# Optimization experiments

Hardware: AMD Instinct MI355X
Metric: run time of the kernel (lower is better)

Reference implementation:

```python
import jax, jax.numpy as jnp
import numpy as np
from jax import lax

E = 20          # num experts / classes
BN_EPS = 1e-5


def _conv(x, w, b=None):
    # NCHW conv, stride 1, 'same' padding (kernel 3x3 or 1x1)
    y = lax.conv_general_dilated(x, w, (1, 1), 'SAME',
                                 dimension_numbers=('NCHW', 'OIHW', 'NCHW'))
    return y if b is None else y + b[None, :, None, None]


def _lrelu(x):
    return jnp.where(x >= 0, x, 0.2 * x)


def _bn(x, g, b, m, v):
    # inference-mode batchnorm
    scale = g * lax.rsqrt(v + BN_EPS)
    return x * scale[None, :, None, None] + (b - m * scale)[None, :, None, None]


def setup_inputs() -> dict:
    key = jax.random.key(0)
    ks = iter(jax.random.split(key, 40))
    def w(shape):
        return jax.random.normal(next(ks), shape, jnp.float32) * 0.05
    d = {}
    d['x'] = jax.random.normal(next(ks), (2, 3, 192, 192), jnp.float32)
    d['noise'] = jax.random.normal(next(ks), (2, 128, 192, 192), jnp.float32)
    # classification head
    d['cls_w1'] = w((64, 3, 3, 3));    d['cls_b1'] = jnp.zeros((64,), jnp.float32)
    d['cls_w2'] = w((128, 64, 3, 3));  d['cls_b2'] = jnp.zeros((128,), jnp.float32)
    d['cls_w3'] = w((256, 128, 3, 3)); d['cls_b3'] = jnp.zeros((256,), jnp.float32)
    d['cls_w4'] = w((512, 256, 1, 1)); d['cls_b4'] = jnp.zeros((512,), jnp.float32)
    d['cls_w5'] = w((E, 512, 1, 1));   d['cls_b5'] = jnp.zeros((E,), jnp.float32)
    for c, i in ((128, 1), (256, 2), (512, 3)):
        d[f'bn{i}_g'] = jnp.ones((c,), jnp.float32)
        d[f'bn{i}_b'] = jnp.zeros((c,), jnp.float32)
        d[f'bn{i}_m'] = jnp.zeros((c,), jnp.float32)
        d[f'bn{i}_v'] = jnp.ones((c,), jnp.float32)
    # 20 expert encoders (stacked on leading axis)
    d['enc_w1'] = w((E, 32, 3, 3, 3));    d['enc_b1'] = jnp.zeros((E, 32), jnp.float32)
    d['enc_w2'] = w((E, 64, 32, 3, 3));   d['enc_b2'] = jnp.zeros((E, 64), jnp.float32)
    d['enc_w3'] = w((E, 128, 64, 3, 3));  d['enc_b3'] = jnp.zeros((E, 128), jnp.float32)
    d['enc_w4'] = w((E, 128, 128, 3, 3)); d['enc_b4'] = jnp.zeros((E, 128), jnp.float32)
    # decoder (legacy=False: first two 1x1 convs have no bias)
    d['dec_w1'] = w((64, 128, 1, 1))
    d['dec_w2'] = w((32, 64, 1, 1))
    d['dec_w3'] = w((3, 32, 1, 1)); d['dec_b3'] = jnp.zeros((3,), jnp.float32)
    return d


def reference(x, noise,
              cls_w1, cls_b1, cls_w2, cls_b2, cls_w3, cls_b3,
              cls_w4, cls_b4, cls_w5, cls_b5,
              bn1_g, bn1_b, bn1_m, bn1_v,
              bn2_g, bn2_b, bn2_m, bn2_v,
              bn3_g, bn3_b, bn3_m, bn3_v,
              enc_w1, enc_b1, enc_w2, enc_b2, enc_w3, enc_b3, enc_w4, enc_b4,
              dec_w1, dec_w2, dec_w3, dec_b3):
    B, _, H, W = x.shape
    C = enc_w4.shape[1]  # 128
    # --- classification / routing ---
    h = _lrelu(_conv(x, cls_w1, cls_b1))
    h = _lrelu(_bn(_conv(h, cls_w2, cls_b2), bn1_g, bn1_b, bn1_m, bn1_v))
    h = _lrelu(_bn(_conv(h, cls_w3, cls_b3), bn2_g, bn2_b, bn2_m, bn2_v))
    h = _lrelu(_bn(_conv(h, cls_w4, cls_b4), bn3_g, bn3_b, bn3_m, bn3_v))
    classes = jax.nn.softmax(_conv(h, cls_w5, cls_b5), axis=1)  # [B,E,H,W]
    idx = jnp.argmax(classes, axis=1)  # [B,H,W] top-1 expert per pixel

    # --- run all 20 dense encoders (faithful to original torch.where masking) ---
    def enc(w1, b1, w2, b2, w3, b3, w4, b4):
        e = _lrelu(_conv(x, w1, b1))
        e = _lrelu(_conv(e, w2, b2))
        e = _lrelu(_conv(e, w3, b3))
        return _conv(e, w4, b4)
    embs = jax.vmap(enc)(enc_w1, enc_b1, enc_w2, enc_b2,
                         enc_w3, enc_b3, enc_w4, enc_b4)  # [E,B,128,H,W]
    embs = jnp.moveaxis(embs, 0, 1)  # [B,E,128,H,W]
    sel_idx = jnp.broadcast_to(idx[:, None, None, :, :], (B, 1, C, H, W))
    emb = jnp.take_along_axis(embs, sel_idx, axis=1)[:, 0]  # [B,128,H,W]

    # --- decode with additive noise ---
    d = _conv(emb + noise, dec_w1)
    d = _conv(d, dec_w2)
    out = _conv(d, dec_w3, dec_b3)  # [B,3,H,W]

    # --- load balancing loss ---
    one_hot = jax.nn.one_hot(idx, E, dtype=jnp.float32)          # [B,H,W,E]
    density = one_hot.reshape(B, -1, E).mean(axis=1)             # [B,E]
    density_proxy = classes.reshape(B, E, -1).mean(axis=-1)      # [B,E]
    lb = (density_proxy * density).mean() * float(E * E)
    return out, lb * 0.1
```

## Files before the change

### kernel.cpp

```cpp
#include <hip/hip_runtime.h>
#include <hip/hip_bf16.h>

typedef __hip_bfloat16 bf16;
typedef unsigned short u16;
typedef short s16x8 __attribute__((ext_vector_type(8)));
typedef float f32x4 __attribute__((ext_vector_type(4)));
#define MFMA16(a, b, c) __builtin_amdgcn_mfma_f32_16x16x32_bf16(a, b, c, 0, 0, 0)

#define HW_   36864
#define WP_   194
#define HWP_  37636
#define W_    192
#define SP_   9216

__device__ __forceinline__ float ldin(const void* p, size_t i, int f32) {
    return f32 ? ((const float*)p)[i] : __bfloat162float(((const bf16*)p)[i]);
}
__device__ __forceinline__ int probe_f32(const void* pr) {
    return ((const unsigned*)pr)[0] == 0x3F800000u;
}
__device__ __forceinline__ u16 f2bf(float f) {
    bf16 h = __float2bfloat16(f);
    return *reinterpret_cast<u16*>(&h);
}

__global__ __launch_bounds__(256) void pad_x_k(const void* __restrict__ x,
                                               float* __restrict__ xpad,
                                               const void* __restrict__ pr) {
    const int f32 = probe_f32(pr);
    int i = blockIdx.x * 256 + threadIdx.x;
    if (i >= 2 * 3 * HW_) return;
    int w = i % W_;
    int h = (i / W_) % W_;
    int c = i / HW_;
    xpad[(size_t)c * HWP_ + (size_t)(h + 1) * WP_ + (w + 1)] = ldin(x, i, f32);
}

__global__ __launch_bounds__(256) void conv3x3_k(
    const float* __restrict__ in, const void* __restrict__ wgt,
    const void* __restrict__ bias, const void* __restrict__ bng,
    const void* __restrict__ bnb, const void* __restrict__ bnm,
    const void* __restrict__ bnv, float* __restrict__ out,
    int Cin, int Cout, int lrelu, const void* __restrict__ pr)
{
    extern __shared__ float wl[];
    const int f32 = probe_f32(pr);
    const int tid = threadIdx.x;
    const int co0 = blockIdx.y * 8;
    const int b   = blockIdx.z;
    const int n = Cin * 72;
    for (int i = tid; i < n; i += 256) {
        int u = i & 7, r = i >> 3;
        int ci = r / 9, tap = r - ci * 9;
        wl[i] = ldin(wgt, ((size_t)(co0 + u) * Cin + ci) * 9 + tap, f32);
    }
    __syncthreads();

    const int pixb = blockIdx.x * 1024 + tid;
    int off[4];
#pragma unroll
    for (int p = 0; p < 4; ++p) {
        int pix = pixb + p * 256;
        int h = pix / W_, w = pix - h * W_;
        off[p] = (h + 1) * WP_ + (w + 1);
    }
    float acc[32];
#pragma unroll
    for (int i = 0; i < 32; ++i) acc[i] = 0.f;

    const int doff[9] = {-(WP_+1), -WP_, -(WP_-1), -1, 0, 1, WP_-1, WP_, WP_+1};
    const float* inb = in + (size_t)b * Cin * HWP_;
    for (int ci = 0; ci < Cin; ++ci) {
        const float* ip = inb + (size_t)ci * HWP_;
        const float* wp = wl + ci * 72;
#pragma unroll
        for (int tap = 0; tap < 9; ++tap) {
            const float4 wa = *(const float4*)(wp + tap * 8);
            const float4 wb = *(const float4*)(wp + tap * 8 + 4);
            const int d = doff[tap];
            float v[4];
#pragma unroll
            for (int p = 0; p < 4; ++p) v[p] = ip[off[p] + d];
#pragma unroll
            for (int p = 0; p < 4; ++p) {
                acc[p*8+0] += v[p] * wa.x;  acc[p*8+1] += v[p] * wa.y;
                acc[p*8+2] += v[p] * wa.z;  acc[p*8+3] += v[p] * wa.w;
                acc[p*8+4] += v[p] * wb.x;  acc[p*8+5] += v[p] * wb.y;
                acc[p*8+6] += v[p] * wb.z;  acc[p*8+7] += v[p] * wb.w;
            }
        }
    }

#pragma unroll
    for (int u = 0; u < 8; ++u) {
        const int co = co0 + u;
        float s = 1.f, t = 0.f;
        if (bng) {
            float g = ldin(bng, co, f32), bb = ldin(bnb, co, f32);
            float m = ldin(bnm, co, f32), vv = ldin(bnv, co, f32);
            s = g * rsqrtf(vv + 1e-5f);
            t = bb - m * s;
        }
        const float bs = bias ? ldin(bias, co, f32) : 0.f;
        float* op = out + ((size_t)b * Cout + co) * HWP_;
#pragma unroll
        for (int p = 0; p < 4; ++p) {
            float val = (acc[p*8+u] + bs) * s + t;
            if (lrelu) val = val >= 0.f ? val : 0.2f * val;
            op[off[p]] = val;
        }
    }
}

__global__ __launch_bounds__(256) void conv1x1s_k(
    const float* __restrict__ in, const void* __restrict__ wgt,
    const void* __restrict__ bias, const void* __restrict__ bng,
    const void* __restrict__ bnb, const void* __restrict__ bnm,
    const void* __restrict__ bnv, float* __restrict__ out,
    int Cin, int pix0, const void* __restrict__ pr)
{
    extern __shared__ float wl[];
    const int f32 = probe_f32(pr);
    const int tid = threadIdx.x;
    const int co0 = blockIdx.y * 8;
    const int b   = blockIdx.z;
    const int n = Cin * 8;
    for (int i = tid; i < n; i += 256) {
        int u = i & 7, ci = i >> 3;
        wl[i] = ldin(wgt, (size_t)(co0 + u) * Cin + ci, f32);
    }
    __syncthreads();

    const int pixb = pix0 + blockIdx.x * 1024 + tid;
    int off[4], lp[4];
#pragma unroll
    for (int p = 0; p < 4; ++p) {
        int pix = pixb + p * 256;
        lp[p] = pix - pix0;
        int h = pix / W_, w = pix - h * W_;
        off[p] = (h + 1) * WP_ + (w + 1);
    }
    float acc[32];
#pragma unroll
    for (int i = 0; i < 32; ++i) acc[i] = 0.f;

    for (int ci = 0; ci < Cin; ++ci) {
        const float* ip = in + ((size_t)b * Cin + ci) * HWP_;
        const float4 wa = *(const float4*)(wl + ci * 8);
        const float4 wb = *(const float4*)(wl + ci * 8 + 4);
        float v[4];
#pragma unroll
        for (int p = 0; p < 4; ++p) v[p] = ip[off[p]];
#pragma unroll
        for (int p = 0; p < 4; ++p) {
            acc[p*8+0] += v[p] * wa.x;  acc[p*8+1] += v[p] * wa.y;
            acc[p*8+2] += v[p] * wa.z;  acc[p*8+3] += v[p] * wa.w;
            acc[p*8+4] += v[p] * wb.x;  acc[p*8+5] += v[p] * wb.y;
            acc[p*8+6] += v[p] * wb.z;  acc[p*8+7] += v[p] * wb.w;
        }
    }

#pragma unroll
    for (int u = 0; u < 8; ++u) {
        const int co = co0 + u;
        float g = ldin(bng, co, f32), bb = ldin(bnb, co, f32);
        float m = ldin(bnm, co, f32), vv = ldin(bnv, co, f32);
        float s = g * rsqrtf(vv + 1e-5f);
        float t = bb - m * s;
        const float bs = ldin(bias, co, f32);
        float* op = out + ((size_t)b * 512 + co) * SP_;
#pragma unroll
        for (int p = 0; p < 4; ++p) {
            float val = (acc[p*8+u] + bs) * s + t;
            val = val >= 0.f ? val : 0.2f * val;
            op[lp[p]] = val;
        }
    }
}

__global__ __launch_bounds__(256) void heads_k(
    const float* __restrict__ c4q, const void* __restrict__ w5,
    const void* __restrict__ b5, int* __restrict__ idx,
    float* __restrict__ proxy, float* __restrict__ cntg, int pix0,
    const void* __restrict__ pr)
{
    extern __shared__ float wl[];
    __shared__ float sums[20];
    __shared__ float cnts[20];
    const int f32 = probe_f32(pr);
    const int tid = threadIdx.x;
    const int b = blockIdx.y;
    for (int i = tid; i < 512 * 20; i += 256) {
        int e = i % 20, ci = i / 20;
        wl[ci * 20 + e] = ldin(w5, (size_t)e * 512 + ci, f32);
    }
    if (tid < 20) { sums[tid] = 0.f; cnts[tid] = 0.f; }
    __syncthreads();

    const int lpix = blockIdx.x * 256 + tid;

    float acc[20];
#pragma unroll
    for (int e = 0; e < 20; ++e) acc[e] = ldin(b5, e, f32);
    const float* ip = c4q + (size_t)b * 512 * SP_;
    for (int ci = 0; ci < 512; ++ci) {
        const float v = ip[(size_t)ci * SP_ + lpix];
        const float* wp = wl + ci * 20;
#pragma unroll
        for (int e = 0; e < 20; ++e) acc[e] += v * wp[e];
    }

    float m = acc[0]; int am = 0;
#pragma unroll
    for (int e = 1; e < 20; ++e) if (acc[e] > m) { m = acc[e]; am = e; }
    float prb[20], ssum = 0.f;
#pragma unroll
    for (int e = 0; e < 20; ++e) { prb[e] = expf(acc[e] - m); ssum += prb[e]; }
    const float inv = 1.f / ssum;
    idx[b * HW_ + pix0 + lpix] = am;

    const int lane = tid & 63;
#pragma unroll
    for (int e = 0; e < 20; ++e) {
        float p = prb[e] * inv;
        p += __shfl_down(p, 32); p += __shfl_down(p, 16); p += __shfl_down(p, 8);
        p += __shfl_down(p, 4);  p += __shfl_down(p, 2);  p += __shfl_down(p, 1);
        if (lane == 0) atomicAdd(&sums[e], p);
        unsigned long long bal = __ballot(am == e);
        if (lane == 0) atomicAdd(&cnts[e], (float)__popcll(bal));
    }
    __syncthreads();
    if (tid < 20) {
        atomicAdd(&proxy[b * 20 + tid], sums[tid]);
        atomicAdd(&cntg[b * 20 + tid], cnts[tid]);
    }
}

__global__ __launch_bounds__(256) void wtx_k(const void* __restrict__ w,
                                             u16* __restrict__ wt,
                                             int Cout, int Cin, int nTot,
                                             const void* __restrict__ pr) {
    const int f32 = probe_f32(pr);
    int i = blockIdx.x * 256 + threadIdx.x;
    if (i >= nTot) return;
    int ci = i % Cin; int r = i / Cin;
    int co = r % Cout; r /= Cout;
    int tap = r % 9; int e = r / 9;
    size_t src = ((size_t)(e * Cout + co) * Cin + ci) * 9 + tap;
    wt[i] = f2bf(ldin(w, src, f32));
}

__global__ __launch_bounds__(512) void fused_expert_k(
    const float* __restrict__ xpad, const int* __restrict__ idx,
    const void* __restrict__ ew1, const void* __restrict__ eb1,
    const u16* __restrict__ Wt2, const void* __restrict__ eb2,
    const u16* __restrict__ Wt3, const void* __restrict__ eb3,
    const u16* __restrict__ Wt4, const void* __restrict__ eb4,
    float* __restrict__ emb, const void* __restrict__ pr)
{
    __shared__ __align__(16) char smem_[137216];
    u16*   e2s = (u16*)smem_;
    u16*   e3s = (u16*)(smem_ + 54272);
    u16*   e1s = (u16*)(smem_ + 54272);
    float* xs  = (float*)smem_;
    float* wl1 = (float*)(smem_ + 6912);
    __shared__ int s_sel[256];
    __shared__ int s_wc[8];

    const int f32 = probe_f32(pr);
    const int tid  = threadIdx.x;
    const int lane = tid & 63, wv = tid >> 6;
    const int ml = lane & 15, q8 = (lane >> 4) * 8, m0 = (lane >> 4) * 4;
    const int b = blockIdx.y;
    const int eid = blockIdx.z;
    const int ty = blockIdx.x / 12, tx = blockIdx.x - ty * 12;
    const int Oh = ty * 16, Ow = tx * 16;

    {
        int sel = 0;
        if (tid < 256) {
            const int r = tid >> 4, c = tid & 15;
            sel = (idx[b * HW_ + (Oh + r) * W_ + (Ow + c)] == eid);
        }
        const unsigned long long m = __ballot(sel);
        if (lane == 0) s_wc[wv] = __popcll(m);
        __syncthreads();
        int cnt = 0;
#pragma unroll
        for (int w = 0; w < 8; ++w) cnt += s_wc[w];
        if (cnt == 0) return;
        int pre = 0;
        for (int w = 0; w < wv; ++w) pre += s_wc[w];
        if (sel)
            s_sel[pre + __popcll(m & ((1ull << lane) - 1ull))] = tid;
    }

    for (int i = tid; i < 24 * 24 * 3; i += 512) {
        int ch = i % 3, pxl = i / 3;
        int r = pxl / 24, c = pxl - r * 24;
        int ir = Oh - 4 + r, ic = Ow - 4 + c;
        float v = 0.f;
        if (ir >= -1 && ir < 193 && ic >= -1 && ic < 193)
            v = xpad[((size_t)b * 3 + ch) * HWP_ + (size_t)(ir + 1) * WP_ + (ic + 1)];
        xs[pxl * 3 + ch] = v;
    }
    for (int i = tid; i < 896; i += 512) {
        if (i < 864) {
            int co = i & 31, k = i >> 5;
            int ci = k / 9, tap = k - ci * 9;
            wl1[i] = ldin(ew1, (size_t)eid * 864 + ((size_t)co * 3 + ci) * 9 + tap, f32);
        } else {
            wl1[i] = ldin(eb1, (size_t)eid * 32 + (i - 864), f32);
        }
    }
    __syncthreads();

    if (tid < 484) {
        const int p = tid;
        const int r1 = p / 22, c1 = p - r1 * 22;
        const int ir = Oh - 3 + r1, ic = Ow - 3 + c1;
        const int inimg = (ir >= 0 && ir < 192 && ic >= 0 && ic < 192);
        float a1[32];
#pragma unroll
        for (int co = 0; co < 32; ++co) a1[co] = 0.f;
        if (inimg) {
#pragma unroll
            for (int ci = 0; ci < 3; ++ci)
#pragma unroll
                for (int tap = 0; tap < 9; ++tap) {
                    const int dy = tap / 3, dx = tap - dy * 3;
                    const float xv = xs[((r1 + dy) * 24 + (c1 + dx)) * 3 + ci];
                    const float* wp = wl1 + (ci * 9 + tap) * 32;
#pragma unroll
                    for (int co = 0; co < 32; ++co) a1[co] += xv * wp[co];
                }
        }
        u16 pk[32];
#pragma unroll
        for (int co = 0; co < 32; ++co) {
            float v = 0.f;
            if (inimg) {
                v = a1[co] + wl1[864 + co];
                v = v >= 0.f ? v : 0.2f * v;
            }
            pk[co] = f2bf(v);
        }
#pragma unroll
        for (int ch = 0; ch < 4; ++ch)
            *(uint4*)(e1s + ((size_t)ch * 488 + p) * 8) = ((const uint4*)pk)[ch];
    }
    __syncthreads();

    {
        const u16* Wt2e = Wt2 + (size_t)eid * 9 * 64 * 32;
        int pxv[4], r2v[4], c2v[4];
#pragma unroll
        for (int j = 0; j < 4; ++j) {
            int t = wv + 8 * j; if (t > 24) t = 24;
            int px = t * 16 + ml;
            pxv[j] = px; r2v[j] = px / 20; c2v[j] = px - (px / 20) * 20;
        }
        f32x4 acc2[4][4];
#pragma unroll
        for (int j = 0; j < 4; ++j)
#pragma unroll
            for (int n = 0; n < 4; ++n) acc2[j][n] = (f32x4){0.f,0.f,0.f,0.f};

#pragma unroll
        for (int tap = 0; tap < 9; ++tap) {
            const int dy = tap / 3, dx = tap - dy * 3;
            s16x8 aW[4];
#pragma unroll
            for (int n = 0; n < 4; ++n)
                aW[n] = *(const s16x8*)(Wt2e + ((size_t)tap * 64 + n * 16 + ml) * 32 + q8);
#pragma unroll
            for (int j = 0; j < 4; ++j) {
                const int lin = (r2v[j] + dy) * 22 + (c2v[j] + dx);
                const s16x8 bA = *(const s16x8*)(e1s + ((size_t)(q8 >> 3) * 488 + lin) * 8);
#pragma unroll
                for (int n = 0; n < 4; ++n) acc2[j][n] = MFMA16(aW[n], bA, acc2[j][n]);
            }
        }
        __syncthreads();
#pragma unroll
        for (int j = 0; j < 4; ++j) {
            const int px = pxv[j];
            const int r2 = r2v[j], c2 = c2v[j];
            const int ir = Oh - 2 + r2, ic = Ow - 2 + c2;
            const int inimg = (ir >= 0 && ir < 192 && ic >= 0 && ic < 192);
#pragma unroll
            for (int n = 0; n < 4; ++n) {
                u16 pk[4];
#pragma unroll
                for (int r = 0; r < 4; ++r) {
                    const int co = n * 16 + m0 + r;
                    float v = 0.f;
                    if (inimg) {
                        v = acc2[j][n][r] + ldin(eb2, (size_t)eid * 64 + co, f32);
                        v = v >= 0.f ? v : 0.2f * v;
                    }
                    pk[r] = f2bf(v);
                }
                const int chunk = (n * 16 + m0) >> 3;
                *(uint2*)(e2s + ((size_t)chunk * 424 + px) * 8 + (m0 & 4)) = *(const uint2*)pk;
            }
        }
    }
    __syncthreads();

    {
        const u16* Wt3e = Wt3 + (size_t)eid * 9 * 128 * 64;
        int pxv[3], r3v[3], c3v[3];
#pragma unroll
        for (int j = 0; j < 3; ++j) {
            int t = wv + 8 * j; if (t > 20) t = 20;
            int px = t * 16 + ml;
            pxv[j] = px; r3v[j] = px / 18; c3v[j] = px - (px / 18) * 18;
        }
#pragma unroll
        for (int np = 0; np < 2; ++np) {
            f32x4 acc3[3][4];
#pragma unroll
            for (int j = 0; j < 3; ++j)
#pragma unroll
                for (int n = 0; n < 4; ++n) acc3[j][n] = (f32x4){0.f,0.f,0.f,0.f};

#pragma unroll
            for (int tap = 0; tap < 9; ++tap) {
                const int dy = tap / 3, dx = tap - dy * 3;
#pragma unroll
                for (int cc = 0; cc < 2; ++cc) {
                    s16x8 aW[4];
#pragma unroll
                    for (int n = 0; n < 4; ++n) {
                        const int co = np * 64 + n * 16 + ml;
                        aW[n] = *(const s16x8*)(Wt3e + ((size_t)tap * 128 + co) * 64 + cc * 32 + q8);
                    }
                    const int chunk = cc * 4 + (q8 >> 3);
#pragma unroll
                    for (int j = 0; j < 3; ++j) {
                        const int lin = (r3v[j] + dy) * 20 + (c3v[j] + dx);
                        const s16x8 bA = *(const s16x8*)(e2s + ((size_t)chunk * 424 + lin) * 8);
#pragma unroll
                        for (int n = 0; n < 4; ++n) acc3[j][n] = MFMA16(aW[n], bA, acc3[j][n]);
                    }
                }
            }
#pragma unroll
            for (int j = 0; j < 3; ++j) {
                const int px = pxv[j];
                if (px >= 324) continue;
                const int r3 = r3v[j], c3 = c3v[j];
                const int ir = Oh - 1 + r3, ic = Ow - 1 + c3;
                const int inimg = (ir >= 0 && ir < 192 && ic >= 0 && ic < 192);
#pragma unroll
                for (int n = 0; n < 4; ++n) {
                    u16 pk[4];
#pragma unroll
                    for (int r = 0; r < 4; ++r) {
                        const int co = np * 64 + n * 16 + m0 + r;
                        float v = 0.f;
                        if (inimg) {
                            v = acc3[j][n][r] + ldin(eb3, (size_t)eid * 128 + co, f32);
                            v = v >= 0.f ? v : 0.2f * v;
                        }
                        pk[r] = f2bf(v);
                    }
                    const int chunk = (np * 64 + n * 16 + m0) >> 3;
                    *(uint2*)(e3s + ((size_t)chunk * 324 + px) * 8 + (m0 & 4)) = *(const uint2*)pk;
                }
            }
        }
    }
    __syncthreads();

    {
        const u16* Wt4e = Wt4 + (size_t)eid * 9 * 128 * 128;
        int cnt = 0;
#pragma unroll
        for (int w = 0; w < 8; ++w) cnt += s_wc[w];
        const int mtiles = (cnt + 15) >> 4;
        const int n0 = wv * 16;
        float bs[4];
#pragma unroll
        for (int r = 0; r < 4; ++r) bs[r] = ldin(eb4, (size_t)eid * 128 + n0 + m0 + r, f32);
        for (int mt = 0; mt < mtiles; ++mt) {
            const int li = mt * 16 + ml;
            const int lpx = (li < cnt) ? s_sel[li] : 0;
            const int rr = lpx >> 4, cc2 = lpx & 15;
            f32x4 acc = {0.f,0.f,0.f,0.f};
#pragma unroll
            for (int tap = 0; tap < 9; ++tap) {
                const int dy = tap / 3, dx = tap - dy * 3;
                const int lin = (rr + dy) * 18 + (cc2 + dx);
#pragma unroll
                for (int c0 = 0; c0 < 128; c0 += 32) {
                    const s16x8 bA = *(const s16x8*)(e3s + ((size_t)((c0 + q8) >> 3) * 324 + lin) * 8);
                    const s16x8 aW = *(const s16x8*)(Wt4e + ((size_t)tap * 128 + n0 + ml) * 128 + c0 + q8);
                    acc = MFMA16(aW, bA, acc);
                }
            }
            if (li < cnt) {
                const int g = (Oh + rr) * W_ + Ow + cc2;
#pragma unroll
                for (int r = 0; r < 4; ++r)
                    emb[((size_t)b * 128 + n0 + m0 + r) * HW_ + g] = acc[r] + bs[r];
            }
        }
    }
}

__global__ __launch_bounds__(256) void dec_fused_k(
    const float* __restrict__ emb, const void* __restrict__ noise,
    const void* __restrict__ dw1, const void* __restrict__ dw2,
    const void* __restrict__ dw3, const void* __restrict__ db3,
    void* __restrict__ outb, const void* __restrict__ pr)
{
    __shared__ float w1s[128 * 64];
    __shared__ float w2s[64 * 32];
    __shared__ float w3s[100];
    const int f32 = probe_f32(pr);
    const int tid = threadIdx.x;
    for (int i = tid; i < 128 * 64; i += 256) {
        int ci = i >> 6, co = i & 63;
        w1s[i] = ldin(dw1, (size_t)co * 128 + ci, f32);
    }
    for (int i = tid; i < 64 * 32; i += 256) {
        int ci = i >> 5, co = i & 31;
        w2s[i] = ldin(dw2, (size_t)co * 64 + ci, f32);
    }
    if (tid < 96) {
        int ci = tid / 3, k = tid - ci * 3;
        w3s[ci * 3 + k] = ldin(dw3, (size_t)k * 32 + ci, f32);
    }
    if (tid >= 96 && tid < 99) w3s[96 + tid - 96] = ldin(db3, tid - 96, f32);
    __syncthreads();

    const int b = blockIdx.y;
    const int pix = blockIdx.x * 256 + tid;

    float h1[64];
#pragma unroll
    for (int i = 0; i < 64; ++i) h1[i] = 0.f;
    for (int ci = 0; ci < 128; ++ci) {
        const size_t base = ((size_t)b * 128 + ci) * HW_ + pix;
        const float v = emb[base] + ldin(noise, base, f32);
        const float* wp = w1s + ci * 64;
#pragma unroll
        for (int c4 = 0; c4 < 16; ++c4) {
            const float4 w = *(const float4*)(wp + c4 * 4);
            h1[c4*4+0] += v * w.x; h1[c4*4+1] += v * w.y;
            h1[c4*4+2] += v * w.z; h1[c4*4+3] += v * w.w;
        }
    }
    float h2[32];
#pragma unroll
    for (int i = 0; i < 32; ++i) h2[i] = 0.f;
#pragma unroll
    for (int ci = 0; ci < 64; ++ci) {
        const float v = h1[ci];
        const float* wp = w2s + ci * 32;
#pragma unroll
        for (int c4 = 0; c4 < 8; ++c4) {
            const float4 w = *(const float4*)(wp + c4 * 4);
            h2[c4*4+0] += v * w.x; h2[c4*4+1] += v * w.y;
            h2[c4*4+2] += v * w.z; h2[c4*4+3] += v * w.w;
        }
    }
    float a0 = w3s[96], a1 = w3s[97], a2 = w3s[98];
#pragma unroll
    for (int ci = 0; ci < 32; ++ci) {
        const float v = h2[ci];
        a0 += v * w3s[ci * 3 + 0];
        a1 += v * w3s[ci * 3 + 1];
        a2 += v * w3s[ci * 3 + 2];
    }
    const size_t o0 = (size_t)(b * 3 + 0) * HW_ + pix;
    const size_t o1 = (size_t)(b * 3 + 1) * HW_ + pix;
    const size_t o2 = (size_t)(b * 3 + 2) * HW_ + pix;
    if (f32) {
        ((float*)outb)[o0] = a0; ((float*)outb)[o1] = a1; ((float*)outb)[o2] = a2;
    } else {
        ((bf16*)outb)[o0] = __float2bfloat16(a0);
        ((bf16*)outb)[o1] = __float2bfloat16(a1);
        ((bf16*)outb)[o2] = __float2bfloat16(a2);
    }
}

__global__ void lb_k(const float* __restrict__ proxy, const float* __restrict__ cnt,
                     void* __restrict__ out, const void* __restrict__ pr) {
    const int f32 = probe_f32(pr);
    const int t = threadIdx.x;
    const float inv = 1.0f / (float)HW_;
    float v = 0.f;
    if (t < 40) v = (proxy[t] * inv) * (cnt[t] * inv);
#pragma unroll
    for (int o = 32; o > 0; o >>= 1) v += __shfl_down(v, o);
    if (t == 0) {
        if (f32) ((float*)out)[221184] = v;
        else     ((bf16*)out)[221184] = __float2bfloat16(v);
    }
}

extern "C" void kernel_launch(void* const* d_in, const int* in_sizes, int n_in,
                              void* d_out, int out_size, void* d_ws, size_t ws_size,
                              hipStream_t stream) {
    (void)in_sizes; (void)n_in; (void)out_size; (void)ws_size;
    const void* x    = d_in[0];
    const void* noise= d_in[1];
    const void* cw1  = d_in[2];  const void* cb1 = d_in[3];
    const void* cw2  = d_in[4];  const void* cb2 = d_in[5];
    const void* cw3  = d_in[6];  const void* cb3 = d_in[7];
    const void* cw4  = d_in[8];  const void* cb4 = d_in[9];
    const void* cw5  = d_in[10]; const void* cb5 = d_in[11];
    const void* bn1g = d_in[12]; const void* bn1b = d_in[13];
    const void* bn1m = d_in[14]; const void* bn1v = d_in[15];
    const void* bn2g = d_in[16]; const void* bn2b = d_in[17];
    const void* bn2m = d_in[18]; const void* bn2v = d_in[19];
    const void* bn3g = d_in[20]; const void* bn3b = d_in[21];
    const void* bn3m = d_in[22]; const void* bn3v = d_in[23];
    const void* ew1  = d_in[24]; const void* eb1 = d_in[25];
    const void* ew2  = d_in[26]; const void* eb2 = d_in[27];
    const void* ew3  = d_in[28]; const void* eb3 = d_in[29];
    const void* ew4  = d_in[30]; const void* eb4 = d_in[31];
    const void* dw1  = d_in[32];
    const void* dw2  = d_in[33];
    const void* dw3  = d_in[34]; const void* db3 = d_in[35];
    const void* pr   = bn1v;

    char* ws = (char*)d_ws;
    constexpr size_t SZ_XPAD = (((size_t)2*3*HWP_*4) + 255) & ~(size_t)255;
    constexpr size_t O_BUF2  = SZ_XPAD;
    constexpr size_t SZ_BUF2 = (size_t)2*256*HWP_*4;
    constexpr size_t O_BUF1  = O_BUF2 + SZ_BUF2;
    constexpr size_t SZ_BUF1 = (size_t)2*128*HWP_*4;
    constexpr size_t O_IDX   = O_BUF1 + SZ_BUF1;
    constexpr size_t O_STAT  = O_IDX + (size_t)2*HW_*4;
    constexpr size_t WS_USED = O_STAT + 512;

    float* xpad  = (float*)(ws);
    float* buf2  = (float*)(ws + O_BUF2);
    int*   idx   = (int*)  (ws + O_IDX);
    float* proxy = (float*)(ws + O_STAT);
    float* cntg  = proxy + 40;

    float* c1  = buf2;
    float* c3  = buf2;
    float* c2  = (float*)(ws + O_BUF1);
    float* c4q = (float*)(ws + O_BUF1);
    float* emb = buf2;
    u16* Wt2 = (u16*)(ws + O_BUF1);
    u16* Wt3 = Wt2 + 368640;
    u16* Wt4 = Wt3 + 1474560;

    hipMemsetAsync(d_ws, 0, WS_USED, stream);

    dim3 blk(256);
    pad_x_k<<<dim3((2*3*HW_ + 255)/256), blk, 0, stream>>>(x, xpad, pr);

    conv3x3_k<<<dim3(36,  8, 2), blk,   3*288, stream>>>(xpad, cw1, cb1, nullptr,nullptr,nullptr,nullptr, c1,   3,  64, 1, pr);
    conv3x3_k<<<dim3(36, 16, 2), blk,  64*288, stream>>>(c1,   cw2, cb2, bn1g,bn1b,bn1m,bn1v,           c2,  64, 128, 1, pr);
    conv3x3_k<<<dim3(36, 32, 2), blk, 128*288, stream>>>(c2,   cw3, cb3, bn2g,bn2b,bn2m,bn2v,           c3, 128, 256, 1, pr);
    for (int s = 0; s < 4; ++s) {
        conv1x1s_k<<<dim3(9, 64, 2), blk, 256*32, stream>>>(c3, cw4, cb4, bn3g,bn3b,bn3m,bn3v, c4q, 256, s*SP_, pr);
        heads_k<<<dim3(36, 2), blk, 512*20*4, stream>>>(c4q, cw5, cb5, idx, proxy, cntg, s*SP_, pr);
    }

    wtx_k<<<dim3(1440),  blk, 0, stream>>>(ew2, Wt2,  64,  32,  368640, pr);
    wtx_k<<<dim3(5760),  blk, 0, stream>>>(ew3, Wt3, 128,  64, 1474560, pr);
    wtx_k<<<dim3(11520), blk, 0, stream>>>(ew4, Wt4, 128, 128, 2949120, pr);

    fused_expert_k<<<dim3(144, 2, 20), dim3(512), 0, stream>>>(
        xpad, idx, ew1, eb1, Wt2, eb2, Wt3, eb3, Wt4, eb4, emb, pr);

    dec_fused_k<<<dim3(144, 2), blk, 0, stream>>>(emb, noise, dw1, dw2, dw3, db3, d_out, pr);
    lb_k<<<1, 64, 0, stream>>>(proxy, cntg, d_out, pr);
}
```

Baseline: 2.816 ms.

## Double fused expert block to 1024 threads, splitting output channels across wave halves

The fused expert kernel now launches 1024 threads per block instead of 512. The two halves of the waves split the work: output channels for conv1, conv2 and conv3, and alternate pixel m-tiles for conv4. Each thread holds fewer accumulators, and twice as many waves share the same ~137KB LDS tile. The aim is to hide latency with more waves per CU, since LDS use limits the block to one per CU. The risks are the register cap from launch_bounds(1024) and redundant B-operand LDS reads, because both halves now load the same activation fragments.

```diff
diff --git a/kernel.cpp b/kernel.cpp
--- a/kernel.cpp
+++ b/kernel.cpp
@@ -250,7 +250,7 @@
     wt[i] = f2bf(ldin(w, src, f32));
 }
 
-__global__ __launch_bounds__(512) void fused_expert_k(
+__global__ __launch_bounds__(1024, 4) void fused_expert_k(
     const float* __restrict__ xpad, const int* __restrict__ idx,
     const void* __restrict__ ew1, const void* __restrict__ eb1,
     const u16* __restrict__ Wt2, const void* __restrict__ eb2,
@@ -265,11 +265,12 @@
     float* xs  = (float*)smem_;
     float* wl1 = (float*)(smem_ + 6912);
     __shared__ int s_sel[256];
-    __shared__ int s_wc[8];
+    __shared__ int s_wc[16];
 
     const int f32 = probe_f32(pr);
     const int tid  = threadIdx.x;
     const int lane = tid & 63, wv = tid >> 6;
+    const int w8 = wv & 7, wn = wv >> 3;
     const int ml = lane & 15, q8 = (lane >> 4) * 8, m0 = (lane >> 4) * 4;
     const int b = blockIdx.y;
     const int eid = blockIdx.z;
@@ -287,7 +288,7 @@
         __syncthreads();
         int cnt = 0;
 #pragma unroll
-        for (int w = 0; w < 8; ++w) cnt += s_wc[w];
+        for (int w = 0; w < 16; ++w) cnt += s_wc[w];
         if (cnt == 0) return;
         int pre = 0;
         for (int w = 0; w < wv; ++w) pre += s_wc[w];
@@ -295,7 +296,7 @@
             s_sel[pre + __popcll(m & ((1ull << lane) - 1ull))] = tid;
     }
 
-    for (int i = tid; i < 24 * 24 * 3; i += 512) {
+    for (int i = tid; i < 24 * 24 * 3; i += 1024) {
         int ch = i % 3, pxl = i / 3;
         int r = pxl / 24, c = pxl - r * 24;
         int ir = Oh - 4 + r, ic = Ow - 4 + c;
@@ -304,7 +305,7 @@
             v = xpad[((size_t)b * 3 + ch) * HWP_ + (size_t)(ir + 1) * WP_ + (ic + 1)];
         xs[pxl * 3 + ch] = v;
     }
-    for (int i = tid; i < 896; i += 512) {
+    for (int i = tid; i < 896; i += 1024) {
         if (i < 864) {
             int co = i & 31, k = i >> 5;
             int ci = k / 9, tap = k - ci * 9;
@@ -315,39 +316,42 @@
     }
     __syncthreads();
 
-    if (tid < 484) {
-        const int p = tid;
-        const int r1 = p / 22, c1 = p - r1 * 22;
-        const int ir = Oh - 3 + r1, ic = Ow - 3 + c1;
-        const int inimg = (ir >= 0 && ir < 192 && ic >= 0 && ic < 192);
-        float a1[32];
-#pragma unroll
-        for (int co = 0; co < 32; ++co) a1[co] = 0.f;
-        if (inimg) {
-#pragma unroll
-            for (int ci = 0; ci < 3; ++ci)
-#pragma unroll
-                for (int tap = 0; tap < 9; ++tap) {
-                    const int dy = tap / 3, dx = tap - dy * 3;
-                    const float xv = xs[((r1 + dy) * 24 + (c1 + dx)) * 3 + ci];
-                    const float* wp = wl1 + (ci * 9 + tap) * 32;
-#pragma unroll
-                    for (int co = 0; co < 32; ++co) a1[co] += xv * wp[co];
+    {
+        const int p   = tid & 511;
+        const int coh = tid >> 9;
+        if (p < 484) {
+            const int r1 = p / 22, c1 = p - r1 * 22;
+            const int ir = Oh - 3 + r1, ic = Ow - 3 + c1;
+            const int inimg = (ir >= 0 && ir < 192 && ic >= 0 && ic < 192);
+            float a1[16];
+#pragma unroll
+            for (int co = 0; co < 16; ++co) a1[co] = 0.f;
+            if (inimg) {
+#pragma unroll
+                for (int ci = 0; ci < 3; ++ci)
+#pragma unroll
+                    for (int tap = 0; tap < 9; ++tap) {
+                        const int dy = tap / 3, dx = tap - dy * 3;
+                        const float xv = xs[((r1 + dy) * 24 + (c1 + dx)) * 3 + ci];
+                        const float* wp = wl1 + (ci * 9 + tap) * 32 + coh * 16;
+#pragma unroll
+                        for (int co = 0; co < 16; ++co) a1[co] += xv * wp[co];
+                    }
+            }
+            u16 pk[16];
+#pragma unroll
+            for (int co = 0; co < 16; ++co) {
+                float v = 0.f;
+                if (inimg) {
+                    v = a1[co] + wl1[864 + coh * 16 + co];
+                    v = v >= 0.f ? v : 0.2f * v;
                 }
-        }
-        u16 pk[32];
-#pragma unroll
-        for (int co = 0; co < 32; ++co) {
-            float v = 0.f;
-            if (inimg) {
-                v = a1[co] + wl1[864 + co];
-                v = v >= 0.f ? v : 0.2f * v;
-            }
-            pk[co] = f2bf(v);
-        }
-#pragma unroll
-        for (int ch = 0; ch < 4; ++ch)
-            *(uint4*)(e1s + ((size_t)ch * 488 + p) * 8) = ((const uint4*)pk)[ch];
+                pk[co] = f2bf(v);
+            }
+#pragma unroll
+            for (int ch = 0; ch < 2; ++ch)
+                *(uint4*)(e1s + ((size_t)(coh * 2 + ch) * 488 + p) * 8) = ((const uint4*)pk)[ch];
+        }
     }
     __syncthreads();
 
@@ -356,29 +360,31 @@
         int pxv[4], r2v[4], c2v[4];
 #pragma unroll
         for (int j = 0; j < 4; ++j) {
-            int t = wv + 8 * j; if (t > 24) t = 24;
+            int t = w8 + 8 * j; if (t > 24) t = 24;
             int px = t * 16 + ml;
             pxv[j] = px; r2v[j] = px / 20; c2v[j] = px - (px / 20) * 20;
         }
-        f32x4 acc2[4][4];
+        f32x4 acc2[4][2];
 #pragma unroll
         for (int j = 0; j < 4; ++j)
 #pragma unroll
-            for (int n = 0; n < 4; ++n) acc2[j][n] = (f32x4){0.f,0.f,0.f,0.f};
+            for (int u = 0; u < 2; ++u) acc2[j][u] = (f32x4){0.f,0.f,0.f,0.f};
 
 #pragma unroll
         for (int tap = 0; tap < 9; ++tap) {
             const int dy = tap / 3, dx = tap - dy * 3;
-            s16x8 aW[4];
-#pragma unroll
-            for (int n = 0; n < 4; ++n)
-                aW[n] = *(const s16x8*)(Wt2e + ((size_t)tap * 64 + n * 16 + ml) * 32 + q8);
+            s16x8 aW[2];
+#pragma unroll
+            for (int u = 0; u < 2; ++u) {
+                const int n = wn * 2 + u;
+                aW[u] = *(const s16x8*)(Wt2e + ((size_t)tap * 64 + n * 16 + ml) * 32 + q8);
+            }
 #pragma unroll
             for (int j = 0; j < 4; ++j) {
                 const int lin = (r2v[j] + dy) * 22 + (c2v[j] + dx);
                 const s16x8 bA = *(const s16x8*)(e1s + ((size_t)(q8 >> 3) * 488 + lin) * 8);
 #pragma unroll
-                for (int n = 0; n < 4; ++n) acc2[j][n] = MFMA16(aW[n], bA, acc2[j][n]);
+                for (int u = 0; u < 2; ++u) acc2[j][u] = MFMA16(aW[u], bA, acc2[j][u]);
             }
         }
         __syncthreads();
@@ -389,14 +395,15 @@
             const int ir = Oh - 2 + r2, ic = Ow - 2 + c2;
             const int inimg = (ir >= 0 && ir < 192 && ic >= 0 && ic < 192);
 #pragma unroll
-            for (int n = 0; n < 4; ++n) {
+            for (int u = 0; u < 2; ++u) {
+                const int n = wn * 2 + u;
                 u16 pk[4];
 #pragma unroll
                 for (int r = 0; r < 4; ++r) {
                     const int co = n * 16 + m0 + r;
                     float v = 0.f;
                     if (inimg) {
-                        v = acc2[j][n][r] + ldin(eb2, (size_t)eid * 64 + co, f32);
+                        v = acc2[j][u][r] + ldin(eb2, (size_t)eid * 64 + co, f32);
                         v = v >= 0.f ? v : 0.2f * v;
                     }
                     pk[r] = f2bf(v);
@@ -410,65 +417,63 @@
 
     {
         const u16* Wt3e = Wt3 + (size_t)eid * 9 * 128 * 64;
+        const int np = wn;
         int pxv[3], r3v[3], c3v[3];
 #pragma unroll
         for (int j = 0; j < 3; ++j) {
-            int t = wv + 8 * j; if (t > 20) t = 20;
+            int t = w8 + 8 * j; if (t > 20) t = 20;
             int px = t * 16 + ml;
             pxv[j] = px; r3v[j] = px / 18; c3v[j] = px - (px / 18) * 18;
         }
-#pragma unroll
-        for (int np = 0; np < 2; ++np) {
-            f32x4 acc3[3][4];
-#pragma unroll
-            for (int j = 0; j < 3; ++j)
-#pragma unroll
-                for (int n = 0; n < 4; ++n) acc3[j][n] = (f32x4){0.f,0.f,0.f,0.f};
-
-#pragma unroll
-            for (int tap = 0; tap < 9; ++tap) {
-                const int dy = tap / 3, dx = tap - dy * 3;
-#pragma unroll
-                for (int cc = 0; cc < 2; ++cc) {
-                    s16x8 aW[4];
-#pragma unroll
-                    for (int n = 0; n < 4; ++n) {
-                        const int co = np * 64 + n * 16 + ml;
-                        aW[n] = *(const s16x8*)(Wt3e + ((size_t)tap * 128 + co) * 64 + cc * 32 + q8);
+        f32x4 acc3[3][4];
+#pragma unroll
+        for (int j = 0; j < 3; ++j)
+#pragma unroll
+            for (int n = 0; n < 4; ++n) acc3[j][n] = (f32x4){0.f,0.f,0.f,0.f};
+
+#pragma unroll
+        for (int tap = 0; tap < 9; ++tap) {
+            const int dy = tap / 3, dx = tap - dy * 3;
+#pragma unroll
+            for (int cc = 0; cc < 2; ++cc) {
+                s16x8 aW[4];
+#pragma unroll
+                for (int n = 0; n < 4; ++n) {
+                    const int co = np * 64 + n * 16 + ml;
+                    aW[n] = *(const s16x8*)(Wt3e + ((size_t)tap * 128 + co) * 64 + cc * 32 + q8);
+                }
+                const int chunk = cc * 4 + (q8 >> 3);
+#pragma unroll
+                for (int j = 0; j < 3; ++j) {
+                    const int lin = (r3v[j] + dy) * 20 + (c3v[j] + dx);
+                    const s16x8 bA = *(const s16x8*)(e2s + ((size_t)chunk * 424 + lin) * 8);
+#pragma unroll
+                    for (int n = 0; n < 4; ++n) acc3[j][n] = MFMA16(aW[n], bA, acc3[j][n]);
+                }
+            }
+        }
+#pragma unroll
+        for (int j = 0; j < 3; ++j) {
+            const int px = pxv[j];
+            if (px >= 324) continue;
+            const int r3 = r3v[j], c3 = c3v[j];
+            const int ir = Oh - 1 + r3, ic = Ow - 1 + c3;
+            const int inimg = (ir >= 0 && ir < 192 && ic >= 0 && ic < 192);
+#pragma unroll
+            for (int n = 0; n < 4; ++n) {
+                u16 pk[4];
+#pragma unroll
+                for (int r = 0; r < 4; ++r) {
+                    const int co = np * 64 + n * 16 + m0 + r;
+                    float v = 0.f;
+                    if (inimg) {
+                        v = acc3[j][n][r] + ldin(eb3, (size_t)eid * 128 + co, f32);
+                        v = v >= 0.f ? v : 0.2f * v;
                     }
-                    const int chunk = cc * 4 + (q8 >> 3);
-#pragma unroll
-                    for (int j = 0; j < 3; ++j) {
-                        const int lin = (r3v[j] + dy) * 20 + (c3v[j] + dx);
-                        const s16x8 bA = *(const s16x8*)(e2s + ((size_t)chunk * 424 + lin) * 8);
-#pragma unroll
-                        for (int n = 0; n < 4; ++n) acc3[j][n] = MFMA16(aW[n], bA, acc3[j][n]);
-                    }
+                    pk[r] = f2bf(v);
                 }
-            }
-#pragma unroll
-            for (int j = 0; j < 3; ++j) {
-                const int px = pxv[j];
-                if (px >= 324) continue;
-                const int r3 = r3v[j], c3 = c3v[j];
-                const int ir = Oh - 1 + r3, ic = Ow - 1 + c3;
-                const int inimg = (ir >= 0 && ir < 192 && ic >= 0 && ic < 192);
-#pragma unroll
-                for (int n = 0; n < 4; ++n) {
-                    u16 pk[4];
-#pragma unroll
-                    for (int r = 0; r < 4; ++r) {
-                        const int co = np * 64 + n * 16 + m0 + r;
-                        float v = 0.f;
-                        if (inimg) {
-                            v = acc3[j][n][r] + ldin(eb3, (size_t)eid * 128 + co, f32);
-                            v = v >= 0.f ? v : 0.2f * v;
-                        }
-                        pk[r] = f2bf(v);
-                    }
-                    const int chunk = (np * 64 + n * 16 + m0) >> 3;
-                    *(uint2*)(e3s + ((size_t)chunk * 324 + px) * 8 + (m0 & 4)) = *(const uint2*)pk;
-                }
+                const int chunk = (np * 64 + n * 16 + m0) >> 3;
+                *(uint2*)(e3s + ((size_t)chunk * 324 + px) * 8 + (m0 & 4)) = *(const uint2*)pk;
             }
         }
     }
@@ -478,13 +483,13 @@
         const u16* Wt4e = Wt4 + (size_t)eid * 9 * 128 * 128;
         int cnt = 0;
 #pragma unroll
-        for (int w = 0; w < 8; ++w) cnt += s_wc[w];
+        for (int w = 0; w < 16; ++w) cnt += s_wc[w];
         const int mtiles = (cnt + 15) >> 4;
-        const int n0 = wv * 16;
+        const int n0 = w8 * 16;
         float bs[4];
 #pragma unroll
         for (int r = 0; r < 4; ++r) bs[r] = ldin(eb4, (size_t)eid * 128 + n0 + m0 + r, f32);
-        for (int mt = 0; mt < mtiles; ++mt) {
+        for (int mt = wn; mt < mtiles; mt += 2) {
             const int li = mt * 16 + ml;
             const int lpx = (li < cnt) ? s_sel[li] : 0;
             const int rr = lpx >> 4, cc2 = lpx & 15;
@@ -670,7 +675,7 @@
     wtx_k<<<dim3(5760),  blk, 0, stream>>>(ew3, Wt3, 128,  64, 1474560, pr);
     wtx_k<<<dim3(11520), blk, 0, stream>>>(ew4, Wt4, 128, 128, 2949120, pr);
 
-    fused_expert_k<<<dim3(144, 2, 20), dim3(512), 0, stream>>>(
+    fused_expert_k<<<dim3(144, 2, 20), dim3(1024), 0, stream>>>(
         xpad, idx, ew1, eb1, Wt2, eb2, Wt3, eb3, Wt4, eb4, emb, pr);
 
     dec_fused_k<<<dim3(144, 2), blk, 0, stream>>>(emb, noise, dw1, dw2, dw3, db3, d_out, pr);
```

After: 2.831 ms. Within noise of the previous version (+0.5%).
